# Kernel optimization log

Measured on AMD Instinct MI355X. Metric: run time of the kernel, lower is better.

The kernel has to match this reference:

```python
import jax, jax.numpy as jnp
import numpy as np

B, T, D, H = 2, 2048, 1024, 16
DK = D // H  # 64


def setup_inputs() -> dict:
    key = jax.random.key(0)
    ks = jax.random.split(key, 8)
    query = jax.random.normal(ks[0], (B, T, D), dtype=jnp.float32)
    key_t = jax.random.normal(ks[1], (B, T, D), dtype=jnp.float32)
    value = jax.random.normal(ks[2], (B, T, D), dtype=jnp.float32)
    # mask: True = blocked (causal), broadcast over batch and heads
    mask = jnp.triu(jnp.ones((T, T), dtype=bool), k=1)[None, None]  # (1,1,T,T)
    # Xavier-uniform Linear weights, torch layout (out_features, in_features)
    lim = float(np.sqrt(6.0 / (D + D)))
    Wq = jax.random.uniform(ks[3], (D, D), minval=-lim, maxval=lim, dtype=jnp.float32)
    Wk = jax.random.uniform(ks[4], (D, D), minval=-lim, maxval=lim, dtype=jnp.float32)
    Wv = jax.random.uniform(ks[5], (D, D), minval=-lim, maxval=lim, dtype=jnp.float32)
    Wo = jax.random.uniform(ks[6], (D, D), minval=-lim, maxval=lim, dtype=jnp.float32)
    return {"query": query, "key": key_t, "value": value, "mask": mask,
            "Wq": Wq, "Wk": Wk, "Wv": Wv, "Wo": Wo}


def _split_heads(x):
    b, t, _ = x.shape
    return x.reshape(b, t, H, DK).transpose(0, 2, 1, 3)  # (B,H,T,DK)


def reference(query, key, value, mask, Wq, Wk, Wv, Wo):
    # torch Linear: x @ W.T
    Q = _split_heads(jnp.einsum('btd,ed->bte', query, Wq))
    K = _split_heads(jnp.einsum('btd,ed->bte', key, Wk))
    V = _split_heads(jnp.einsum('btd,ed->bte', value, Wv))
    scale = jnp.sqrt(jnp.float32(DK))
    scores = jnp.einsum('bhqd,bhkd->bhqk', Q, K) / scale  # (B,H,Tq,Tk)
    scores = jnp.where(mask, jnp.float32(-1e9), scores)
    attn_weights = jax.nn.softmax(scores, axis=-1)
    attn_weights = jnp.nan_to_num(attn_weights, nan=0.0)
    attn_out = jnp.einsum('bhqk,bhkd->bhqd', attn_weights, V)  # (B,H,Tq,DK)
    combined = attn_out.transpose(0, 2, 1, 3).reshape(query.shape[0], -1, D)
    output = jnp.einsum('btd,ed->bte', combined, Wo)
    return output, attn_weights
```

## Files before the change

### kernel.cpp

```cpp
#include <hip/hip_runtime.h>
#include <hip/hip_bf16.h>
#include <stdint.h>

#define Bx  2
#define Tx  2048
#define Dx  1024
#define Hx  16
#define DKx 64

typedef unsigned short u16;
typedef short bf16x8 __attribute__((ext_vector_type(8)));
typedef float f32x4 __attribute__((ext_vector_type(4)));

#define QKVE ((size_t)Bx * Tx * Dx)
#define WEL  ((size_t)Dx * Dx)

static __device__ __forceinline__ u16 f32_to_bf16(float f) {
  union { float f; unsigned u; } v; v.f = f;
  unsigned r = v.u + 0x7fffu + ((v.u >> 16) & 1u);
  return (u16)(r >> 16);
}

static __device__ __forceinline__ void gld_lds16(const u16* g, u16* l) {
  __builtin_amdgcn_global_load_lds(
      (__attribute__((address_space(1))) const unsigned int*)g,
      (__attribute__((address_space(3))) unsigned int*)l, 16, 0, 0);
}

template <int ROWS, int COLS, bool SWZ>
static __device__ __forceinline__ void stage_lds_b16(const u16* __restrict__ g,
                                                     int gstride, u16* lds) {
  constexpr int CPR = COLS / 8;
  constexpr int TOTAL = ROWS * CPR;
  const int lane = threadIdx.x & 63;
  const int wb = threadIdx.x & ~63;
#pragma unroll
  for (int base = 0; base < TOTAL; base += 256) {
    const int c = base + wb + lane;
    const int r = c / CPR;
    int sl = c % CPR;
    if (SWZ) sl ^= (r & (CPR - 1));
    gld_lds16(g + (size_t)r * gstride + sl * 8, lds + (size_t)(base + wb) * 8);
  }
}

template <int ROWS, int COLS>
static __device__ __forceinline__ void stage_tile_f32(const float* __restrict__ g,
                                                      int gstride, u16* lds) {
  constexpr int CPR = COLS / 4;
  constexpr int TOTAL = ROWS * CPR;
  const int tid = threadIdx.x;
#pragma unroll
  for (int base = 0; base < TOTAL; base += 256) {
    int c = base + tid;
    int r = c / CPR;
    int cc = c % CPR;
    float4 v = *(const float4*)(g + (size_t)r * gstride + cc * 4);
    ushort4 p;
    p.x = f32_to_bf16(v.x);
    p.y = f32_to_bf16(v.y);
    p.z = f32_to_bf16(v.z);
    p.w = f32_to_bf16(v.w);
    *(ushort4*)&lds[(size_t)r * COLS + cc * 4] = p;
  }
}

__global__ __launch_bounds__(256) void cvt_kernel(
    const float* __restrict__ q, const float* __restrict__ k,
    const float* __restrict__ v, const float* __restrict__ wq,
    const float* __restrict__ wk, const float* __restrict__ wv,
    u16* __restrict__ dst) {
  const size_t total4 = (3 * QKVE + 3 * WEL) / 4;
  for (size_t i = (size_t)blockIdx.x * blockDim.x + threadIdx.x; i < total4;
       i += (size_t)gridDim.x * blockDim.x) {
    size_t e = i * 4;
    const float* src;
    size_t off;
    if (e < 3 * QKVE) {
      int w = (int)(e >> 22);
      src = (w == 0) ? q : (w == 1) ? k : v;
      off = e - ((size_t)w << 22);
    } else {
      size_t e2 = e - 3 * QKVE;
      int w = (int)(e2 >> 20);
      src = (w == 0) ? wq : (w == 1) ? wk : wv;
      off = e2 - ((size_t)w << 20);
    }
    float4 x = *(const float4*)(src + off);
    ushort4 p;
    p.x = f32_to_bf16(x.x);
    p.y = f32_to_bf16(x.y);
    p.z = f32_to_bf16(x.z);
    p.w = f32_to_bf16(x.w);
    *(ushort4*)(dst + e) = p;
  }
}

__global__ __launch_bounds__(256) void gemm_qkv(
    const u16* __restrict__ cvt, u16* __restrict__ Qp,
    u16* __restrict__ Kp, u16* __restrict__ Vtp) {
  __shared__ u16 As[128 * 64];
  __shared__ u16 Bs[128 * 64];
  const int z = blockIdx.z;
  const u16* A = cvt + (size_t)z * QKVE;
  const u16* W = cvt + 3 * QKVE + (size_t)z * WEL;
  u16* dst = (z == 0) ? Qp : (z == 1) ? Kp : Vtp;
  const int K = Dx;
  const int tid = threadIdx.x;
  const int lane = tid & 63;
  const int l15 = lane & 15;
  const int quad = lane >> 4;
  const int wave = tid >> 6;
  const int m0 = blockIdx.y * 128;
  const int n0 = blockIdx.x * 128;
  const int wr = (wave >> 1) * 64;
  const int wc = (wave & 1) * 64;

  f32x4 acc[4][4];
#pragma unroll
  for (int i = 0; i < 4; i++)
#pragma unroll
    for (int j = 0; j < 4; j++) acc[i][j] = f32x4{0.f, 0.f, 0.f, 0.f};

  for (int k0 = 0; k0 < K; k0 += 64) {
    stage_lds_b16<128, 64, false>(A + (size_t)m0 * K + k0, K, As);
    stage_lds_b16<128, 64, false>(W + (size_t)n0 * K + k0, K, Bs);
    __syncthreads();
#pragma unroll
    for (int kk = 0; kk < 2; kk++) {
      bf16x8 af[4], bfv[4];
#pragma unroll
      for (int i = 0; i < 4; i++)
        af[i] = *(const bf16x8*)&As[(wr + i * 16 + l15) * 64 + kk * 32 + quad * 8];
#pragma unroll
      for (int j = 0; j < 4; j++)
        bfv[j] = *(const bf16x8*)&Bs[(wc + j * 16 + l15) * 64 + kk * 32 + quad * 8];
#pragma unroll
      for (int i = 0; i < 4; i++)
#pragma unroll
        for (int j = 0; j < 4; j++)
          acc[i][j] = __builtin_amdgcn_mfma_f32_16x16x32_bf16(af[i], bfv[j],
                                                              acc[i][j], 0, 0, 0);
    }
    __syncthreads();
  }

#pragma unroll
  for (int i = 0; i < 4; i++)
#pragma unroll
    for (int j = 0; j < 4; j++)
#pragma unroll
      for (int r = 0; r < 4; r++) {
        int row = m0 + wr + i * 16 + quad * 4 + r;
        int col = n0 + wc + j * 16 + l15;
        float fv = acc[i][j][r];
        int b = row >> 11, t = row & 2047;
        int h = col >> 6, dk = col & 63;
        if (z != 2) {
          dst[(((size_t)(b * Hx + h) * Tx) + t) * DKx + dk] = f32_to_bf16(fv);
        } else {
          dst[(((size_t)(b * Hx + h) * DKx) + dk) * Tx + t] = f32_to_bf16(fv);
        }
      }
}

__global__ __launch_bounds__(256) void gemm_out(
    const u16* __restrict__ Acomb, const float* __restrict__ Wo,
    float* __restrict__ out) {
  __shared__ u16 As[128 * 64];
  __shared__ u16 Bs[128 * 64];
  const int K = Dx, N = Dx;
  const int tid = threadIdx.x;
  const int lane = tid & 63;
  const int l15 = lane & 15;
  const int quad = lane >> 4;
  const int wave = tid >> 6;
  const int m0 = blockIdx.y * 128;
  const int n0 = blockIdx.x * 128;
  const int wr = (wave >> 1) * 64;
  const int wc = (wave & 1) * 64;

  f32x4 acc[4][4];
#pragma unroll
  for (int i = 0; i < 4; i++)
#pragma unroll
    for (int j = 0; j < 4; j++) acc[i][j] = f32x4{0.f, 0.f, 0.f, 0.f};

  for (int k0 = 0; k0 < K; k0 += 64) {
    stage_lds_b16<128, 64, false>(Acomb + (size_t)m0 * K + k0, K, As);
    stage_tile_f32<128, 64>(Wo + (size_t)n0 * K + k0, K, Bs);
    __syncthreads();
#pragma unroll
    for (int kk = 0; kk < 2; kk++) {
      bf16x8 af[4], bfv[4];
#pragma unroll
      for (int i = 0; i < 4; i++)
        af[i] = *(const bf16x8*)&As[(wr + i * 16 + l15) * 64 + kk * 32 + quad * 8];
#pragma unroll
      for (int j = 0; j < 4; j++)
        bfv[j] = *(const bf16x8*)&Bs[(wc + j * 16 + l15) * 64 + kk * 32 + quad * 8];
#pragma unroll
      for (int i = 0; i < 4; i++)
#pragma unroll
        for (int j = 0; j < 4; j++)
          acc[i][j] = __builtin_amdgcn_mfma_f32_16x16x32_bf16(af[i], bfv[j],
                                                              acc[i][j], 0, 0, 0);
    }
    __syncthreads();
  }

#pragma unroll
  for (int i = 0; i < 4; i++)
#pragma unroll
    for (int j = 0; j < 4; j++)
#pragma unroll
      for (int r = 0; r < 4; r++) {
        int row = m0 + wr + i * 16 + quad * 4 + r;
        int col = n0 + wc + j * 16 + l15;
        __builtin_nontemporal_store(acc[i][j][r], &out[(size_t)row * N + col]);
      }
}

__global__ __launch_bounds__(256, 4) void attn_kernel(
    const u16* __restrict__ Q,
    const u16* __restrict__ Kt,
    const u16* __restrict__ Vt,
    float* __restrict__ attnW,
    u16* __restrict__ comb) {
  __shared__ u16 Ks[2][64 * 64];
  __shared__ u16 Vs[2][64 * 64];
  __shared__ u16 Ps[4][16 * 64];

  const int tid = threadIdx.x, lane = tid & 63, wave = tid >> 6;
  const int l15 = lane & 15, quad = lane >> 4;
  const int bh = blockIdx.y;
  const int b = bh >> 4, h = bh & 15;
  const int qb = blockIdx.x;
  const int q0 = qb * 64;
  const u16* Qbh = Q + (size_t)bh * Tx * DKx;
  const u16* Kbh = Kt + (size_t)bh * Tx * DKx;
  const u16* Vbh = Vt + (size_t)bh * DKx * Tx;
  float* Wbh = attnW + (size_t)bh * Tx * Tx;

  bf16x8 qf[2];
  {
    const u16* qrow = Qbh + (size_t)(q0 + wave * 16 + l15) * DKx;
    qf[0] = *(const bf16x8*)(qrow + quad * 8);
    qf[1] = *(const bf16x8*)(qrow + 32 + quad * 8);
  }
  const int myrow_base = q0 + wave * 16;
  const float scale = 0.125f;

  float lsum[4];
#pragma unroll
  for (int r = 0; r < 4; r++) lsum[r] = 0.0f;

  stage_lds_b16<64, 64, true>(Kbh, DKx, Ks[0]);
  __syncthreads();
  for (int kt = 0; kt <= qb; kt++) {
    const int cur = kt & 1;
    if (kt < qb)
      stage_lds_b16<64, 64, true>(Kbh + (size_t)(kt + 1) * 64 * DKx, DKx,
                                  Ks[cur ^ 1]);
    f32x4 s[4];
#pragma unroll
    for (int j = 0; j < 4; j++) s[j] = f32x4{0.f, 0.f, 0.f, 0.f};
#pragma unroll
    for (int kk = 0; kk < 2; kk++)
#pragma unroll
      for (int j = 0; j < 4; j++) {
        int krow = j * 16 + l15;
        bf16x8 bfr = *(const bf16x8*)&Ks[cur][(krow * 64 + kk * 32 + quad * 8) ^
                                             ((krow & 7) << 3)];
        s[j] = __builtin_amdgcn_mfma_f32_16x16x32_bf16(qf[kk], bfr, s[j], 0, 0, 0);
      }
    if (kt < qb) {
#pragma unroll
      for (int r = 0; r < 4; r++)
#pragma unroll
        for (int j = 0; j < 4; j++) lsum[r] += __expf(s[j][r] * scale);
    } else {
#pragma unroll
      for (int r = 0; r < 4; r++) {
        int row = myrow_base + quad * 4 + r;
#pragma unroll
        for (int j = 0; j < 4; j++) {
          int col = q0 + j * 16 + l15;
          lsum[r] += (col <= row) ? __expf(s[j][r] * scale) : 0.0f;
        }
      }
    }
    __syncthreads();
  }

  float il[4];
#pragma unroll
  for (int r = 0; r < 4; r++) {
#pragma unroll
    for (int off = 1; off < 16; off <<= 1)
      lsum[r] += __shfl_xor(lsum[r], off);
    il[r] = 1.0f / lsum[r];
  }

  f32x4 o[4];
#pragma unroll
  for (int j = 0; j < 4; j++) o[j] = f32x4{0.f, 0.f, 0.f, 0.f};

  u16* Pw = Ps[wave];

  stage_lds_b16<64, 64, true>(Kbh, DKx, Ks[0]);
  stage_lds_b16<64, 64, true>(Vbh, Tx, Vs[0]);
  __syncthreads();
  for (int kt = 0; kt <= qb; kt++) {
    const int cur = kt & 1;
    if (kt < qb) {
      stage_lds_b16<64, 64, true>(Kbh + (size_t)(kt + 1) * 64 * DKx, DKx,
                                  Ks[cur ^ 1]);
      stage_lds_b16<64, 64, true>(Vbh + (size_t)(kt + 1) * 64, Tx, Vs[cur ^ 1]);
    }
    f32x4 s[4];
#pragma unroll
    for (int j = 0; j < 4; j++) s[j] = f32x4{0.f, 0.f, 0.f, 0.f};
#pragma unroll
    for (int kk = 0; kk < 2; kk++)
#pragma unroll
      for (int j = 0; j < 4; j++) {
        int krow = j * 16 + l15;
        bf16x8 bfr = *(const bf16x8*)&Ks[cur][(krow * 64 + kk * 32 + quad * 8) ^
                                             ((krow & 7) << 3)];
        s[j] = __builtin_amdgcn_mfma_f32_16x16x32_bf16(qf[kk], bfr, s[j], 0, 0, 0);
      }
    if (kt < qb) {
#pragma unroll
      for (int j = 0; j < 4; j++)
#pragma unroll
        for (int r = 0; r < 4; r++) {
          int row = myrow_base + quad * 4 + r;
          int col = kt * 64 + j * 16 + l15;
          float p = __expf(s[j][r] * scale) * il[r];
          int prow = quad * 4 + r;
          Pw[(prow * 64 + j * 16 + l15) ^ ((prow & 7) << 3)] = f32_to_bf16(p);
          __builtin_nontemporal_store(p, &Wbh[(size_t)row * Tx + col]);
        }
    } else {
#pragma unroll
      for (int j = 0; j < 4; j++)
#pragma unroll
        for (int r = 0; r < 4; r++) {
          int row = myrow_base + quad * 4 + r;
          int col = q0 + j * 16 + l15;
          float p = (col <= row) ? __expf(s[j][r] * scale) * il[r] : 0.0f;
          int prow = quad * 4 + r;
          Pw[(prow * 64 + j * 16 + l15) ^ ((prow & 7) << 3)] = f32_to_bf16(p);
          __builtin_nontemporal_store(p, &Wbh[(size_t)row * Tx + col]);
        }
    }
#pragma unroll
    for (int kk = 0; kk < 2; kk++) {
      bf16x8 af = *(const bf16x8*)&Pw[(l15 * 64 + kk * 32 + quad * 8) ^
                                      ((l15 & 7) << 3)];
#pragma unroll
      for (int j = 0; j < 4; j++) {
        int vrow = j * 16 + l15;
        bf16x8 bfr = *(const bf16x8*)&Vs[cur][(vrow * 64 + kk * 32 + quad * 8) ^
                                             ((vrow & 7) << 3)];
        o[j] = __builtin_amdgcn_mfma_f32_16x16x32_bf16(af, bfr, o[j], 0, 0, 0);
      }
    }
    __syncthreads();
  }

  {
    const int c0 = (qb + 1) * 64;
    f32x4 z = {0.f, 0.f, 0.f, 0.f};
#pragma unroll
    for (int rr = 0; rr < 16; rr++) {
      float* dst = &Wbh[(size_t)(myrow_base + rr) * Tx];
      for (int c = c0 + lane * 4; c < Tx; c += 256)
        __builtin_nontemporal_store(z, (f32x4*)&dst[c]);
    }
  }

#pragma unroll
  for (int j = 0; j < 4; j++)
#pragma unroll
    for (int r = 0; r < 4; r++) {
      int row = myrow_base + quad * 4 + r;
      int dk = j * 16 + l15;
      comb[((size_t)b * Tx + row) * Dx + h * 64 + dk] = f32_to_bf16(o[j][r]);
    }
}

extern "C" void kernel_launch(void* const* d_in, const int* in_sizes, int n_in,
                              void* d_out, int out_size, void* d_ws, size_t ws_size,
                              hipStream_t stream) {
  const float* q  = (const float*)d_in[0];
  const float* k  = (const float*)d_in[1];
  const float* v  = (const float*)d_in[2];
  const float* Wq = (const float*)d_in[4];
  const float* Wk = (const float*)d_in[5];
  const float* Wv = (const float*)d_in[6];
  const float* Wo = (const float*)d_in[7];

  float* out  = (float*)d_out;
  float* attn = out + QKVE;

  u16* ws = (u16*)d_ws;
  const size_t QKV = QKVE;
  u16* Qp   = ws;
  u16* Kp   = ws + QKV;
  u16* Vtp  = ws + 2 * QKV;
  u16* comb = ws + 3 * QKV;

  u16* cvt = (u16*)attn;

  dim3 blk(256);
  cvt_kernel<<<dim3(1024), blk, 0, stream>>>(q, k, v, Wq, Wk, Wv, cvt);

  dim3 g1(Dx / 128, (Bx * Tx) / 128, 3);
  gemm_qkv<<<g1, blk, 0, stream>>>(cvt, Qp, Kp, Vtp);

  dim3 g2(Tx / 64, Bx * Hx);
  attn_kernel<<<g2, blk, 0, stream>>>(Qp, Kp, Vtp, attn, comb);

  dim3 g3(Dx / 128, (Bx * Tx) / 128);
  gemm_out<<<g3, blk, 0, stream>>>(comb, Wo, out);
}
```

Measured before the change: 796.8 us.

## Pair causal query tiles per block to balance attention work and share K/V loads

```diff
diff --git a/kernel.cpp b/kernel.cpp
--- a/kernel.cpp
+++ b/kernel.cpp
@@ -221,7 +221,7 @@
       }
 }
 
-__global__ __launch_bounds__(256, 4) void attn_kernel(
+__global__ __launch_bounds__(256, 2) void attn_kernel(
     const u16* __restrict__ Q,
     const u16* __restrict__ Kt,
     const u16* __restrict__ Vt,
@@ -235,159 +235,239 @@
   const int l15 = lane & 15, quad = lane >> 4;
   const int bh = blockIdx.y;
   const int b = bh >> 4, h = bh & 15;
-  const int qb = blockIdx.x;
-  const int q0 = qb * 64;
+  const int p = blockIdx.x;
+  const int qA = p;
+  const int qB = (Tx / 64 - 1) - p;
+  const int nt = qB + 1;
   const u16* Qbh = Q + (size_t)bh * Tx * DKx;
   const u16* Kbh = Kt + (size_t)bh * Tx * DKx;
   const u16* Vbh = Vt + (size_t)bh * DKx * Tx;
   float* Wbh = attnW + (size_t)bh * Tx * Tx;
 
-  bf16x8 qf[2];
+  bf16x8 qfA[2], qfB[2];
   {
-    const u16* qrow = Qbh + (size_t)(q0 + wave * 16 + l15) * DKx;
-    qf[0] = *(const bf16x8*)(qrow + quad * 8);
-    qf[1] = *(const bf16x8*)(qrow + 32 + quad * 8);
-  }
-  const int myrow_base = q0 + wave * 16;
+    const u16* qr = Qbh + (size_t)(qA * 64 + wave * 16 + l15) * DKx;
+    qfA[0] = *(const bf16x8*)(qr + quad * 8);
+    qfA[1] = *(const bf16x8*)(qr + 32 + quad * 8);
+    qr = Qbh + (size_t)(qB * 64 + wave * 16 + l15) * DKx;
+    qfB[0] = *(const bf16x8*)(qr + quad * 8);
+    qfB[1] = *(const bf16x8*)(qr + 32 + quad * 8);
+  }
+  const int rbA = qA * 64 + wave * 16;
+  const int rbB = qB * 64 + wave * 16;
   const float scale = 0.125f;
 
-  float lsum[4];
-#pragma unroll
-  for (int r = 0; r < 4; r++) lsum[r] = 0.0f;
+  float lsA[4], lsB[4];
+#pragma unroll
+  for (int r = 0; r < 4; r++) { lsA[r] = 0.0f; lsB[r] = 0.0f; }
 
   stage_lds_b16<64, 64, true>(Kbh, DKx, Ks[0]);
   __syncthreads();
-  for (int kt = 0; kt <= qb; kt++) {
+  for (int kt = 0; kt < nt; kt++) {
     const int cur = kt & 1;
-    if (kt < qb)
+    if (kt + 1 < nt)
       stage_lds_b16<64, 64, true>(Kbh + (size_t)(kt + 1) * 64 * DKx, DKx,
                                   Ks[cur ^ 1]);
-    f32x4 s[4];
-#pragma unroll
-    for (int j = 0; j < 4; j++) s[j] = f32x4{0.f, 0.f, 0.f, 0.f};
-#pragma unroll
-    for (int kk = 0; kk < 2; kk++)
-#pragma unroll
-      for (int j = 0; j < 4; j++) {
-        int krow = j * 16 + l15;
-        bf16x8 bfr = *(const bf16x8*)&Ks[cur][(krow * 64 + kk * 32 + quad * 8) ^
-                                             ((krow & 7) << 3)];
-        s[j] = __builtin_amdgcn_mfma_f32_16x16x32_bf16(qf[kk], bfr, s[j], 0, 0, 0);
+    {
+      f32x4 s[4];
+#pragma unroll
+      for (int j = 0; j < 4; j++) s[j] = f32x4{0.f, 0.f, 0.f, 0.f};
+#pragma unroll
+      for (int kk = 0; kk < 2; kk++)
+#pragma unroll
+        for (int j = 0; j < 4; j++) {
+          int krow = j * 16 + l15;
+          bf16x8 bfr = *(const bf16x8*)&Ks[cur][(krow * 64 + kk * 32 + quad * 8) ^
+                                               ((krow & 7) << 3)];
+          s[j] = __builtin_amdgcn_mfma_f32_16x16x32_bf16(qfB[kk], bfr, s[j], 0, 0, 0);
+        }
+      if (kt < qB) {
+#pragma unroll
+        for (int r = 0; r < 4; r++)
+#pragma unroll
+          for (int j = 0; j < 4; j++) lsB[r] += __expf(s[j][r] * scale);
+      } else {
+#pragma unroll
+        for (int r = 0; r < 4; r++) {
+          int row = rbB + quad * 4 + r;
+#pragma unroll
+          for (int j = 0; j < 4; j++) {
+            int col = kt * 64 + j * 16 + l15;
+            lsB[r] += (col <= row) ? __expf(s[j][r] * scale) : 0.0f;
+          }
+        }
       }
-    if (kt < qb) {
-#pragma unroll
-      for (int r = 0; r < 4; r++)
-#pragma unroll
-        for (int j = 0; j < 4; j++) lsum[r] += __expf(s[j][r] * scale);
-    } else {
-#pragma unroll
-      for (int r = 0; r < 4; r++) {
-        int row = myrow_base + quad * 4 + r;
+    }
+    if (kt <= qA) {
+      f32x4 s[4];
+#pragma unroll
+      for (int j = 0; j < 4; j++) s[j] = f32x4{0.f, 0.f, 0.f, 0.f};
+#pragma unroll
+      for (int kk = 0; kk < 2; kk++)
 #pragma unroll
         for (int j = 0; j < 4; j++) {
-          int col = q0 + j * 16 + l15;
-          lsum[r] += (col <= row) ? __expf(s[j][r] * scale) : 0.0f;
+          int krow = j * 16 + l15;
+          bf16x8 bfr = *(const bf16x8*)&Ks[cur][(krow * 64 + kk * 32 + quad * 8) ^
+                                               ((krow & 7) << 3)];
+          s[j] = __builtin_amdgcn_mfma_f32_16x16x32_bf16(qfA[kk], bfr, s[j], 0, 0, 0);
+        }
+      if (kt < qA) {
+#pragma unroll
+        for (int r = 0; r < 4; r++)
+#pragma unroll
+          for (int j = 0; j < 4; j++) lsA[r] += __expf(s[j][r] * scale);
+      } else {
+#pragma unroll
+        for (int r = 0; r < 4; r++) {
+          int row = rbA + quad * 4 + r;
+#pragma unroll
+          for (int j = 0; j < 4; j++) {
+            int col = kt * 64 + j * 16 + l15;
+            lsA[r] += (col <= row) ? __expf(s[j][r] * scale) : 0.0f;
+          }
         }
       }
     }
     __syncthreads();
   }
 
-  float il[4];
+  float ilA[4], ilB[4];
 #pragma unroll
   for (int r = 0; r < 4; r++) {
 #pragma unroll
-    for (int off = 1; off < 16; off <<= 1)
-      lsum[r] += __shfl_xor(lsum[r], off);
-    il[r] = 1.0f / lsum[r];
-  }
-
-  f32x4 o[4];
-#pragma unroll
-  for (int j = 0; j < 4; j++) o[j] = f32x4{0.f, 0.f, 0.f, 0.f};
+    for (int off = 1; off < 16; off <<= 1) {
+      lsA[r] += __shfl_xor(lsA[r], off);
+      lsB[r] += __shfl_xor(lsB[r], off);
+    }
+    ilA[r] = 1.0f / lsA[r];
+    ilB[r] = 1.0f / lsB[r];
+  }
+
+  f32x4 oA[4], oB[4];
+#pragma unroll
+  for (int j = 0; j < 4; j++) {
+    oA[j] = f32x4{0.f, 0.f, 0.f, 0.f};
+    oB[j] = f32x4{0.f, 0.f, 0.f, 0.f};
+  }
 
   u16* Pw = Ps[wave];
 
   stage_lds_b16<64, 64, true>(Kbh, DKx, Ks[0]);
   stage_lds_b16<64, 64, true>(Vbh, Tx, Vs[0]);
   __syncthreads();
-  for (int kt = 0; kt <= qb; kt++) {
+  for (int kt = 0; kt < nt; kt++) {
     const int cur = kt & 1;
-    if (kt < qb) {
+    if (kt + 1 < nt) {
       stage_lds_b16<64, 64, true>(Kbh + (size_t)(kt + 1) * 64 * DKx, DKx,
                                   Ks[cur ^ 1]);
       stage_lds_b16<64, 64, true>(Vbh + (size_t)(kt + 1) * 64, Tx, Vs[cur ^ 1]);
     }
-    f32x4 s[4];
-#pragma unroll
-    for (int j = 0; j < 4; j++) s[j] = f32x4{0.f, 0.f, 0.f, 0.f};
-#pragma unroll
-    for (int kk = 0; kk < 2; kk++)
-#pragma unroll
-      for (int j = 0; j < 4; j++) {
-        int krow = j * 16 + l15;
-        bf16x8 bfr = *(const bf16x8*)&Ks[cur][(krow * 64 + kk * 32 + quad * 8) ^
-                                             ((krow & 7) << 3)];
-        s[j] = __builtin_amdgcn_mfma_f32_16x16x32_bf16(qf[kk], bfr, s[j], 0, 0, 0);
+    {
+      f32x4 s[4];
+#pragma unroll
+      for (int j = 0; j < 4; j++) s[j] = f32x4{0.f, 0.f, 0.f, 0.f};
+#pragma unroll
+      for (int kk = 0; kk < 2; kk++)
+#pragma unroll
+        for (int j = 0; j < 4; j++) {
+          int krow = j * 16 + l15;
+          bf16x8 bfr = *(const bf16x8*)&Ks[cur][(krow * 64 + kk * 32 + quad * 8) ^
+                                               ((krow & 7) << 3)];
+          s[j] = __builtin_amdgcn_mfma_f32_16x16x32_bf16(qfB[kk], bfr, s[j], 0, 0, 0);
+        }
+#pragma unroll
+      for (int j = 0; j < 4; j++)
+#pragma unroll
+        for (int r = 0; r < 4; r++) {
+          int row = rbB + quad * 4 + r;
+          int col = kt * 64 + j * 16 + l15;
+          float pv = (kt < qB || col <= row) ? __expf(s[j][r] * scale) * ilB[r]
+                                             : 0.0f;
+          int prow = quad * 4 + r;
+          Pw[(prow * 64 + j * 16 + l15) ^ ((prow & 7) << 3)] = f32_to_bf16(pv);
+          __builtin_nontemporal_store(pv, &Wbh[(size_t)row * Tx + col]);
+        }
+#pragma unroll
+      for (int kk = 0; kk < 2; kk++) {
+        bf16x8 af = *(const bf16x8*)&Pw[(l15 * 64 + kk * 32 + quad * 8) ^
+                                        ((l15 & 7) << 3)];
+#pragma unroll
+        for (int j = 0; j < 4; j++) {
+          int vrow = j * 16 + l15;
+          bf16x8 bfr = *(const bf16x8*)&Vs[cur][(vrow * 64 + kk * 32 + quad * 8) ^
+                                               ((vrow & 7) << 3)];
+          oB[j] = __builtin_amdgcn_mfma_f32_16x16x32_bf16(af, bfr, oB[j], 0, 0, 0);
+        }
       }
-    if (kt < qb) {
+    }
+    if (kt <= qA) {
+      f32x4 s[4];
+#pragma unroll
+      for (int j = 0; j < 4; j++) s[j] = f32x4{0.f, 0.f, 0.f, 0.f};
+#pragma unroll
+      for (int kk = 0; kk < 2; kk++)
+#pragma unroll
+        for (int j = 0; j < 4; j++) {
+          int krow = j * 16 + l15;
+          bf16x8 bfr = *(const bf16x8*)&Ks[cur][(krow * 64 + kk * 32 + quad * 8) ^
+                                               ((krow & 7) << 3)];
+          s[j] = __builtin_amdgcn_mfma_f32_16x16x32_bf16(qfA[kk], bfr, s[j], 0, 0, 0);
+        }
 #pragma unroll
       for (int j = 0; j < 4; j++)
 #pragma unroll
         for (int r = 0; r < 4; r++) {
-          int row = myrow_base + quad * 4 + r;
+          int row = rbA + quad * 4 + r;
           int col = kt * 64 + j * 16 + l15;
-          float p = __expf(s[j][r] * scale) * il[r];
+          float pv = (kt < qA || col <= row) ? __expf(s[j][r] * scale) * ilA[r]
+                                             : 0.0f;
           int prow = quad * 4 + r;
-          Pw[(prow * 64 + j * 16 + l15) ^ ((prow & 7) << 3)] = f32_to_bf16(p);
-          __builtin_nontemporal_store(p, &Wbh[(size_t)row * Tx + col]);
-        }
-    } else {
-#pragma unroll
-      for (int j = 0; j < 4; j++)
-#pragma unroll
-        for (int r = 0; r < 4; r++) {
-          int row = myrow_base + quad * 4 + r;
-          int col = q0 + j * 16 + l15;
-          float p = (col <= row) ? __expf(s[j][r] * scale) * il[r] : 0.0f;
-          int prow = quad * 4 + r;
-          Pw[(prow * 64 + j * 16 + l15) ^ ((prow & 7) << 3)] = f32_to_bf16(p);
-          __builtin_nontemporal_store(p, &Wbh[(size_t)row * Tx + col]);
-        }
-    }
-#pragma unroll
-    for (int kk = 0; kk < 2; kk++) {
-      bf16x8 af = *(const bf16x8*)&Pw[(l15 * 64 + kk * 32 + quad * 8) ^
-                                      ((l15 & 7) << 3)];
-#pragma unroll
-      for (int j = 0; j < 4; j++) {
-        int vrow = j * 16 + l15;
-        bf16x8 bfr = *(const bf16x8*)&Vs[cur][(vrow * 64 + kk * 32 + quad * 8) ^
-                                             ((vrow & 7) << 3)];
-        o[j] = __builtin_amdgcn_mfma_f32_16x16x32_bf16(af, bfr, o[j], 0, 0, 0);
+          Pw[(prow * 64 + j * 16 + l15) ^ ((prow & 7) << 3)] = f32_to_bf16(pv);
+          __builtin_nontemporal_store(pv, &Wbh[(size_t)row * Tx + col]);
+        }
+#pragma unroll
+      for (int kk = 0; kk < 2; kk++) {
+        bf16x8 af = *(const bf16x8*)&Pw[(l15 * 64 + kk * 32 + quad * 8) ^
+                                        ((l15 & 7) << 3)];
+#pragma unroll
+        for (int j = 0; j < 4; j++) {
+          int vrow = j * 16 + l15;
+          bf16x8 bfr = *(const bf16x8*)&Vs[cur][(vrow * 64 + kk * 32 + quad * 8) ^
+                                               ((vrow & 7) << 3)];
+          oA[j] = __builtin_amdgcn_mfma_f32_16x16x32_bf16(af, bfr, oA[j], 0, 0, 0);
+        }
       }
     }
     __syncthreads();
   }
 
   {
-    const int c0 = (qb + 1) * 64;
     f32x4 z = {0.f, 0.f, 0.f, 0.f};
+    const int cA = (qA + 1) * 64;
 #pragma unroll
     for (int rr = 0; rr < 16; rr++) {
-      float* dst = &Wbh[(size_t)(myrow_base + rr) * Tx];
-      for (int c = c0 + lane * 4; c < Tx; c += 256)
+      float* dst = &Wbh[(size_t)(rbA + rr) * Tx];
+      for (int c = cA + lane * 4; c < Tx; c += 256)
         __builtin_nontemporal_store(z, (f32x4*)&dst[c]);
     }
+    const int cB = (qB + 1) * 64;
+#pragma unroll
+    for (int rr = 0; rr < 16; rr++) {
+      float* dst = &Wbh[(size_t)(rbB + rr) * Tx];
+      for (int c = cB + lane * 4; c < Tx; c += 256)
+        __builtin_nontemporal_store(z, (f32x4*)&dst[c]);
+    }
   }
 
 #pragma unroll
   for (int j = 0; j < 4; j++)
 #pragma unroll
     for (int r = 0; r < 4; r++) {
-      int row = myrow_base + quad * 4 + r;
       int dk = j * 16 + l15;
-      comb[((size_t)b * Tx + row) * Dx + h * 64 + dk] = f32_to_bf16(o[j][r]);
+      int rowA = rbA + quad * 4 + r;
+      comb[((size_t)b * Tx + rowA) * Dx + h * 64 + dk] = f32_to_bf16(oA[j][r]);
+      int rowB = rbB + quad * 4 + r;
+      comb[((size_t)b * Tx + rowB) * Dx + h * 64 + dk] = f32_to_bf16(oB[j][r]);
     }
 }
 
@@ -420,7 +500,7 @@
   dim3 g1(Dx / 128, (Bx * Tx) / 128, 3);
   gemm_qkv<<<g1, blk, 0, stream>>>(cvt, Qp, Kp, Vtp);
 
-  dim3 g2(Tx / 64, Bx * Hx);
+  dim3 g2(Tx / 128, Bx * Hx);
   attn_kernel<<<g2, blk, 0, stream>>>(Qp, Kp, Vtp, attn, comb);
 
   dim3 g3(Dx / 128, (Bx * Tx) / 128);
```

Result: no change. 798.8 us (+0.3%).
